# Kernel optimization log

Measured on AMD Instinct MI355X. Metric: run time of the kernel, lower is better.

## Reference

```python
import jax, jax.numpy as jnp
import numpy as np

EMBED_DIM = 256
NUM_HEADS = 8
HEAD_WIDTH = 32
B, L = 2, 2048


def setup_inputs() -> dict:
    key = jax.random.key(0)
    k1, k2, k3, k4 = jax.random.split(key, 4)
    x = jax.random.normal(k1, (B, L, EMBED_DIM), dtype=jnp.float32)
    bias = jax.random.normal(k2, (B, L, L, NUM_HEADS), dtype=jnp.float32)
    # torch Linear weights: [out_features, in_features]
    W_proj = jax.random.normal(k3, (3 * EMBED_DIM, EMBED_DIM), dtype=jnp.float32) * (EMBED_DIM ** -0.5)
    W_o = jax.random.normal(k4, (EMBED_DIM, EMBED_DIM), dtype=jnp.float32) * (EMBED_DIM ** -0.5)
    b_o = jnp.zeros((EMBED_DIM,), dtype=jnp.float32)
    return {"x": x, "bias": bias, "W_proj": W_proj, "W_o": W_o, "b_o": b_o}


def reference(x, bias, W_proj, W_o, b_o):
    b, l, _ = x.shape
    h, hw = NUM_HEADS, HEAD_WIDTH
    # fused QKV projection: (b, l, 3*E)
    t = jnp.einsum('ble,fe->blf', x, W_proj)
    # rearrange '... l (h c) -> ... h l c' with c = 3*hw, then split
    t = t.reshape(b, l, h, 3 * hw).transpose(0, 2, 1, 3)  # (b, h, l, 3*hw)
    q, k, v = jnp.split(t, 3, axis=-1)
    q = q * (hw ** -0.5)
    a = jnp.einsum('bhqc,bhkc->bhqk', q, k)
    a = a + bias.transpose(0, 3, 1, 2)  # (b, h, lq, lk)
    a = jax.nn.softmax(a, axis=-1)
    y = jnp.einsum('bhqk,bhkc->bqhc', a, v)
    y = y.reshape(b, l, h * hw)
    return jnp.einsum('ble,fe->blf', y, W_o) + b_o
```

## Files before the change

### kernel.cpp

```cpp
#include <hip/hip_runtime.h>
#include <math.h>

#define NH   8
#define HW   32
#define LSEQ 2048
#define EMB  256
#define BB   2

typedef short bf16x8 __attribute__((ext_vector_type(8)));
typedef float f32x4  __attribute__((ext_vector_type(4)));

__device__ __forceinline__ unsigned short f2bf(float x) {
  union { float f; unsigned u; } v; v.f = x;
  unsigned r = v.u + 0x7fffu + ((v.u >> 16) & 1u);
  return (unsigned short)(r >> 16);
}
__device__ __forceinline__ float bf2f(unsigned short h) {
  union { float f; unsigned u; } v; v.u = ((unsigned)h) << 16;
  return v.f;
}
__device__ __forceinline__ void split2(float x, unsigned short& h, unsigned short& l) {
  h = f2bf(x);
  l = f2bf(x - bf2f(h));
}

__global__ __launch_bounds__(256, 4) void qkv_gemm(
    const float* __restrict__ X, const float* __restrict__ Wp,
    unsigned short* __restrict__ Qh, unsigned short* __restrict__ Ql,
    unsigned short* __restrict__ Kh, unsigned short* __restrict__ Kl,
    unsigned short* __restrict__ Vth, unsigned short* __restrict__ Vtl) {
  const int t = threadIdx.x;
  const int w = t >> 6, lane = t & 63;
  const int col = lane & 15, quad = lane >> 4;
  const int m0 = blockIdx.y * 64 + w * 16;
  const int n0 = blockIdx.x * 64;
  const float* xrow = X + (size_t)(m0 + col) * 256 + quad * 8;

  f32x4 acc[4];
#pragma unroll
  for (int nt = 0; nt < 4; ++nt) acc[nt] = (f32x4){0.f, 0.f, 0.f, 0.f};

#pragma unroll
  for (int es = 0; es < 8; ++es) {
    float4 xa = *(const float4*)(xrow + es * 32);
    float4 xb = *(const float4*)(xrow + es * 32 + 4);
    float xv[8] = {xa.x, xa.y, xa.z, xa.w, xb.x, xb.y, xb.z, xb.w};
    bf16x8 ah, al;
#pragma unroll
    for (int j = 0; j < 8; ++j) {
      unsigned short hi, lo; split2(xv[j], hi, lo);
      ah[j] = (short)hi; al[j] = (short)lo;
    }
#pragma unroll
    for (int nt = 0; nt < 4; ++nt) {
      const float* wrow = Wp + (size_t)(n0 + nt * 16 + col) * 256 + es * 32 + quad * 8;
      float4 wa = *(const float4*)(wrow);
      float4 wb = *(const float4*)(wrow + 4);
      float wv[8] = {wa.x, wa.y, wa.z, wa.w, wb.x, wb.y, wb.z, wb.w};
      bf16x8 bh, bl;
#pragma unroll
      for (int j = 0; j < 8; ++j) {
        unsigned short hi, lo; split2(wv[j], hi, lo);
        bh[j] = (short)hi; bl[j] = (short)lo;
      }
      acc[nt] = __builtin_amdgcn_mfma_f32_16x16x32_bf16(ah, bh, acc[nt], 0, 0, 0);
      acc[nt] = __builtin_amdgcn_mfma_f32_16x16x32_bf16(ah, bl, acc[nt], 0, 0, 0);
      acc[nt] = __builtin_amdgcn_mfma_f32_16x16x32_bf16(al, bh, acc[nt], 0, 0, 0);
    }
  }

  const float qscale = 0.17677669529663687f;
#pragma unroll
  for (int nt = 0; nt < 4; ++nt) {
    const int f = n0 + nt * 16 + col;
    const int hd = f / 96, r0 = f - hd * 96;
#pragma unroll
    for (int r = 0; r < 4; ++r) {
      const int m = m0 + quad * 4 + r;
      const int bbv = m >> 11, ll = m & 2047;
      float v = acc[nt][r];
      unsigned short hi, lo;
      if (r0 < 64) {
        float sv = (r0 < 32) ? v * qscale : v;
        split2(sv, hi, lo);
        size_t idx = ((size_t)(bbv * NH + hd) * LSEQ + ll) * HW + (r0 & 31);
        if (r0 < 32) { Qh[idx] = hi; Ql[idx] = lo; }
        else         { Kh[idx] = hi; Kl[idx] = lo; }
      } else {
        split2(v, hi, lo);
        size_t idx = ((size_t)(bbv * NH + hd) * HW + (r0 - 64)) * LSEQ + ll;
        Vth[idx] = hi; Vtl[idx] = lo;
      }
    }
  }
}

__global__ __launch_bounds__(512, 4) void attn(
    const unsigned short* __restrict__ Qh, const unsigned short* __restrict__ Ql,
    const unsigned short* __restrict__ Kh, const unsigned short* __restrict__ Kl,
    const unsigned short* __restrict__ Vth, const unsigned short* __restrict__ Vtl,
    const float* __restrict__ Bias, float* __restrict__ Yp,
    float* __restrict__ Mm, float* __restrict__ Ll) {
  __shared__ __attribute__((aligned(16))) float Bst[4 * 32 * 72];
  __shared__ __attribute__((aligned(16))) float Pbuf[8 * 1152];
  const int t = threadIdx.x;
  const int w = t >> 6, lane = t & 63;
  const int col = lane & 15, quad = lane >> 4;
  const int head = w >> 1, wks = w & 1;
  const int x = blockIdx.x;
  const int p = ((x >> 4) << 3) | (x & 7);
  const int hh = (x >> 3) & 1;
  const int ks = p & 1;
  const int b = (p >> 1) & 1;
  const int q0g = (p >> 2) * 32;
  const int hg = hh * 4 + head;
  const int kbase = ks * 1024;

  const size_t bhoff = (size_t)(b * NH + hg) * LSEQ * HW;
  const unsigned short* Qhp = Qh + bhoff;
  const unsigned short* Qlp = Ql + bhoff;
  const unsigned short* Khp = Kh + bhoff;
  const unsigned short* Klp = Kl + bhoff;
  const unsigned short* Vhp = Vth + bhoff;
  const unsigned short* Vlp = Vtl + bhoff;
  float* Pw = &Pbuf[w * 1152];

  bf16x8 Qbh[2], Qbl[2];
#pragma unroll
  for (int qt = 0; qt < 2; ++qt) {
    size_t off = (size_t)(q0g + qt * 16 + col) * HW + quad * 8;
    Qbh[qt] = *(const bf16x8*)(Qhp + off);
    Qbl[qt] = *(const bf16x8*)(Qlp + off);
  }

  f32x4 o[2][2];
#pragma unroll
  for (int ct = 0; ct < 2; ++ct)
#pragma unroll
    for (int qt = 0; qt < 2; ++qt) o[ct][qt] = (f32x4){0.f, 0.f, 0.f, 0.f};
  float m_i[2] = {-1e30f, -1e30f}, l_i[2] = {0.f, 0.f};

  const int sq = w, sk = lane;
  float4 bsr[4];
#pragma unroll
  for (int u = 0; u < 4; ++u)
    bsr[u] = *(const float4*)&Bias[(((size_t)(b * LSEQ + q0g + u * 8 + sq)) * LSEQ +
                                    kbase + sk) * NH + hh * 4];

#pragma unroll 1
  for (int it = 0; it < 16; ++it) {
    __syncthreads();
#pragma unroll
    for (int u = 0; u < 4; ++u) {
      const int qq = u * 8 + sq;
      Bst[0 * 2304 + qq * 72 + sk] = bsr[u].x;
      Bst[1 * 2304 + qq * 72 + sk] = bsr[u].y;
      Bst[2 * 2304 + qq * 72 + sk] = bsr[u].z;
      Bst[3 * 2304 + qq * 72 + sk] = bsr[u].w;
    }
    const int kw = kbase + it * 64 + wks * 32;
    bf16x8 Kah[2], Kal[2], Vah[2], Val[2];
#pragma unroll
    for (int kt = 0; kt < 2; ++kt) {
      size_t off = (size_t)(kw + kt * 16 + col) * HW + quad * 8;
      Kah[kt] = *(const bf16x8*)(Khp + off);
      Kal[kt] = *(const bf16x8*)(Klp + off);
    }
#pragma unroll
    for (int ct = 0; ct < 2; ++ct) {
      size_t off = (size_t)(ct * 16 + col) * LSEQ + kw + quad * 8;
      Vah[ct] = *(const bf16x8*)(Vhp + off);
      Val[ct] = *(const bf16x8*)(Vlp + off);
    }
    if (it < 15) {
#pragma unroll
      for (int u = 0; u < 4; ++u)
        bsr[u] = *(const float4*)&Bias[(((size_t)(b * LSEQ + q0g + u * 8 + sq)) * LSEQ +
                                        kbase + (it + 1) * 64 + sk) * NH + hh * 4];
    }
    __syncthreads();

    f32x4 s[2][2];
#pragma unroll
    for (int kt = 0; kt < 2; ++kt)
#pragma unroll
      for (int qt = 0; qt < 2; ++qt) {
        f32x4 a = *(const f32x4*)&Bst[head * 2304 + (qt * 16 + col) * 72 +
                                      wks * 32 + kt * 16 + quad * 4];
        a = __builtin_amdgcn_mfma_f32_16x16x32_bf16(Kah[kt], Qbh[qt], a, 0, 0, 0);
        a = __builtin_amdgcn_mfma_f32_16x16x32_bf16(Kah[kt], Qbl[qt], a, 0, 0, 0);
        a = __builtin_amdgcn_mfma_f32_16x16x32_bf16(Kal[kt], Qbh[qt], a, 0, 0, 0);
        s[kt][qt] = a;
      }

    float alpha[2];
#pragma unroll
    for (int qt = 0; qt < 2; ++qt) {
      float mx = s[0][qt][0];
#pragma unroll
      for (int r = 1; r < 4; ++r) mx = fmaxf(mx, s[0][qt][r]);
#pragma unroll
      for (int r = 0; r < 4; ++r) mx = fmaxf(mx, s[1][qt][r]);
      mx = fmaxf(mx, __shfl_xor(mx, 16, 64));
      mx = fmaxf(mx, __shfl_xor(mx, 32, 64));
      float mnew = fmaxf(m_i[qt], mx);
      float al = __expf(m_i[qt] - mnew);
      float ps = 0.f;
#pragma unroll
      for (int kt = 0; kt < 2; ++kt)
#pragma unroll
        for (int r = 0; r < 4; ++r) {
          float pv = __expf(s[kt][qt][r] - mnew);
          s[kt][qt][r] = pv;
          ps += pv;
        }
      ps += __shfl_xor(ps, 16, 64);
      ps += __shfl_xor(ps, 32, 64);
      l_i[qt] = l_i[qt] * al + ps;
      m_i[qt] = mnew;
      alpha[qt] = al;
#pragma unroll
      for (int ct = 0; ct < 2; ++ct)
#pragma unroll
        for (int r = 0; r < 4; ++r) o[ct][qt][r] *= al;
    }

#pragma unroll
    for (int kt = 0; kt < 2; ++kt)
#pragma unroll
      for (int qt = 0; qt < 2; ++qt)
#pragma unroll
        for (int r = 0; r < 4; ++r)
          Pw[(kt * 16 + quad * 4 + r) * 34 + qt * 16 + col] = s[kt][qt][r];
    bf16x8 Pbh[2], Pbl[2];
#pragma unroll
    for (int qt = 0; qt < 2; ++qt) {
#pragma unroll
      for (int j = 0; j < 8; ++j) {
        float pv = Pw[(quad * 8 + j) * 34 + qt * 16 + col];
        unsigned short hi, lo; split2(pv, hi, lo);
        Pbh[qt][j] = (short)hi; Pbl[qt][j] = (short)lo;
      }
    }
#pragma unroll
    for (int ct = 0; ct < 2; ++ct)
#pragma unroll
      for (int qt = 0; qt < 2; ++qt) {
        f32x4 a = o[ct][qt];
        a = __builtin_amdgcn_mfma_f32_16x16x32_bf16(Vah[ct], Pbh[qt], a, 0, 0, 0);
        a = __builtin_amdgcn_mfma_f32_16x16x32_bf16(Vah[ct], Pbl[qt], a, 0, 0, 0);
        a = __builtin_amdgcn_mfma_f32_16x16x32_bf16(Val[ct], Pbh[qt], a, 0, 0, 0);
        o[ct][qt] = a;
      }
  }

  __syncthreads();
  if (wks == 1) {
#pragma unroll
    for (int ct = 0; ct < 2; ++ct)
#pragma unroll
      for (int qt = 0; qt < 2; ++qt)
#pragma unroll
        for (int r = 0; r < 4; ++r)
          Pw[(ct * 16 + quad * 4 + r) * 34 + qt * 16 + col] = o[ct][qt][r];
    if (quad == 0) {
#pragma unroll
      for (int qt = 0; qt < 2; ++qt) {
        Pw[1088 + qt * 16 + col] = m_i[qt];
        Pw[1120 + qt * 16 + col] = l_i[qt];
      }
    }
  }
  __syncthreads();
  if (wks == 0) {
    const float* Pp = Pw + 1152;
#pragma unroll
    for (int qt = 0; qt < 2; ++qt) {
      float m2 = Pp[1088 + qt * 16 + col];
      float l2 = Pp[1120 + qt * 16 + col];
      float mm = fmaxf(m_i[qt], m2);
      float a1 = __expf(m_i[qt] - mm);
      float a2 = __expf(m2 - mm);
      float lm = l_i[qt] * a1 + l2 * a2;
      const size_t row = (size_t)ks * 4096 + b * LSEQ + q0g + qt * 16 + col;
      if (quad == 0) {
        Mm[row * 8 + hg] = mm;
        Ll[row * 8 + hg] = lm;
      }
#pragma unroll
      for (int ct = 0; ct < 2; ++ct) {
        float4 res;
        res.x = o[ct][qt][0] * a1 + Pp[(ct * 16 + quad * 4 + 0) * 34 + qt * 16 + col] * a2;
        res.y = o[ct][qt][1] * a1 + Pp[(ct * 16 + quad * 4 + 1) * 34 + qt * 16 + col] * a2;
        res.z = o[ct][qt][2] * a1 + Pp[(ct * 16 + quad * 4 + 2) * 34 + qt * 16 + col] * a2;
        res.w = o[ct][qt][3] * a1 + Pp[(ct * 16 + quad * 4 + 3) * 34 + qt * 16 + col] * a2;
        *(float4*)&Yp[row * EMB + hg * HW + ct * 16 + quad * 4] = res;
      }
    }
  }
}

__global__ __launch_bounds__(256, 4) void out_gemm(
    const float* __restrict__ Yp, const float* __restrict__ Mm,
    const float* __restrict__ Ll, const float* __restrict__ Wo,
    const float* __restrict__ bo, float* __restrict__ Out) {
  const int t = threadIdx.x;
  const int w = t >> 6, lane = t & 63;
  const int col = lane & 15, quad = lane >> 4;
  const int m0 = blockIdx.y * 64 + w * 16;
  const int n0 = blockIdx.x * 64;
  const int grow = m0 + col;
  const float* o1p = Yp + (size_t)grow * 256 + quad * 8;
  const float* o2p = o1p + (size_t)4096 * 256;

  f32x4 acc[4];
#pragma unroll
  for (int nt = 0; nt < 4; ++nt) acc[nt] = (f32x4){0.f, 0.f, 0.f, 0.f};

#pragma unroll
  for (int es = 0; es < 8; ++es) {
    float m1 = Mm[(size_t)grow * 8 + es];
    float l1 = Ll[(size_t)grow * 8 + es];
    float m2 = Mm[(size_t)(4096 + grow) * 8 + es];
    float l2 = Ll[(size_t)(4096 + grow) * 8 + es];
    float M = fmaxf(m1, m2);
    float w1 = __expf(m1 - M), w2 = __expf(m2 - M);
    float inv = 1.0f / (l1 * w1 + l2 * w2);
    w1 *= inv; w2 *= inv;
    float4 a1 = *(const float4*)(o1p + es * 32);
    float4 b1 = *(const float4*)(o1p + es * 32 + 4);
    float4 a2 = *(const float4*)(o2p + es * 32);
    float4 b2 = *(const float4*)(o2p + es * 32 + 4);
    float yv[8] = {a1.x * w1 + a2.x * w2, a1.y * w1 + a2.y * w2,
                   a1.z * w1 + a2.z * w2, a1.w * w1 + a2.w * w2,
                   b1.x * w1 + b2.x * w2, b1.y * w1 + b2.y * w2,
                   b1.z * w1 + b2.z * w2, b1.w * w1 + b2.w * w2};
    bf16x8 ah, al;
#pragma unroll
    for (int j = 0; j < 8; ++j) {
      unsigned short hi, lo; split2(yv[j], hi, lo);
      ah[j] = (short)hi; al[j] = (short)lo;
    }
#pragma unroll
    for (int nt = 0; nt < 4; ++nt) {
      const float* wrow = Wo + (size_t)(n0 + nt * 16 + col) * 256 + es * 32 + quad * 8;
      float4 wa = *(const float4*)(wrow);
      float4 wb = *(const float4*)(wrow + 4);
      float wv[8] = {wa.x, wa.y, wa.z, wa.w, wb.x, wb.y, wb.z, wb.w};
      bf16x8 bh, bl;
#pragma unroll
      for (int j = 0; j < 8; ++j) {
        unsigned short hi, lo; split2(wv[j], hi, lo);
        bh[j] = (short)hi; bl[j] = (short)lo;
      }
      acc[nt] = __builtin_amdgcn_mfma_f32_16x16x32_bf16(ah, bh, acc[nt], 0, 0, 0);
      acc[nt] = __builtin_amdgcn_mfma_f32_16x16x32_bf16(ah, bl, acc[nt], 0, 0, 0);
      acc[nt] = __builtin_amdgcn_mfma_f32_16x16x32_bf16(al, bh, acc[nt], 0, 0, 0);
    }
  }
#pragma unroll
  for (int nt = 0; nt < 4; ++nt) {
    const int f = n0 + nt * 16 + col;
    const float bias_o = bo[f];
#pragma unroll
    for (int r = 0; r < 4; ++r)
      Out[(size_t)(m0 + quad * 4 + r) * 256 + f] = acc[nt][r] + bias_o;
  }
}

extern "C" void kernel_launch(void* const* d_in, const int* in_sizes, int n_in,
                              void* d_out, int out_size, void* d_ws, size_t ws_size,
                              hipStream_t stream) {
  const float* X    = (const float*)d_in[0];
  const float* Bias = (const float*)d_in[1];
  const float* Wp   = (const float*)d_in[2];
  const float* Wo   = (const float*)d_in[3];
  const float* bo   = (const float*)d_in[4];
  float* Out = (float*)d_out;

  const size_t qkv_elems = (size_t)BB * NH * LSEQ * HW;
  unsigned short* Qh  = (unsigned short*)d_ws;
  unsigned short* Ql  = Qh + qkv_elems;
  unsigned short* Kh  = Ql + qkv_elems;
  unsigned short* Kl  = Kh + qkv_elems;
  unsigned short* Vth = Kl + qkv_elems;
  unsigned short* Vtl = Vth + qkv_elems;
  float* Yp = (float*)(Vtl + qkv_elems);
  float* Mm = Yp + (size_t)2 * 4096 * 256;
  float* Ll = Mm + (size_t)2 * 4096 * 8;

  qkv_gemm<<<dim3(12, 64), 256, 0, stream>>>(X, Wp, Qh, Ql, Kh, Kl, Vth, Vtl);
  attn<<<dim3(512), 512, 0, stream>>>(Qh, Ql, Kh, Kl, Vth, Vtl, Bias, Yp, Mm, Ll);
  out_gemm<<<dim3(4, 64), 256, 0, stream>>>(Yp, Mm, Ll, Wo, bo, Out);
}
```

Before: 458.1 us.

## Presplit inputs and weights to bf16 hi/lo once, store P pre-split in LDS

Adds a presplit kernel that converts X, W_proj and W_o into bf16 hi/lo pairs once, so the GEMM kernels load ready-made bf16 vectors instead of redoing the split for every tile. In attention, P is split before being written to LDS as packed hi/lo, and the K/V global loads are issued before the bias LDS stores. out_gemm loads m/l with vector loads hoisted out of the loop. The cost is an extra kernel launch and extra workspace traffic for the split copies.

Result: faster. 448.8 us (-2.0%).

```diff
diff --git a/kernel.cpp b/kernel.cpp
--- a/kernel.cpp
+++ b/kernel.cpp
@@ -9,6 +9,7 @@
 
 typedef short bf16x8 __attribute__((ext_vector_type(8)));
 typedef float f32x4  __attribute__((ext_vector_type(4)));
+typedef unsigned short u16x4 __attribute__((ext_vector_type(4)));
 
 __device__ __forceinline__ unsigned short f2bf(float x) {
   union { float f; unsigned u; } v; v.f = x;
@@ -24,8 +25,37 @@
   l = f2bf(x - bf2f(h));
 }
 
+__global__ __launch_bounds__(256) void presplit(
+    const float* __restrict__ X, const float* __restrict__ Wp,
+    const float* __restrict__ Wo,
+    unsigned short* __restrict__ Xh, unsigned short* __restrict__ Xl,
+    unsigned short* __restrict__ Wph, unsigned short* __restrict__ Wpl,
+    unsigned short* __restrict__ Woh, unsigned short* __restrict__ Wol) {
+  const int NX = 4096 * 256, NP = 768 * 256, NO = 256 * 256;
+  const int total4 = (NX + NP + NO) >> 2;
+  int i4 = blockIdx.x * 256 + threadIdx.x;
+  if (i4 >= total4) return;
+  int e = i4 << 2;
+  const float* src;
+  unsigned short *dh, *dl;
+  int off;
+  if (e < NX)           { src = X;  dh = Xh;  dl = Xl;  off = e; }
+  else if (e < NX + NP) { src = Wp; dh = Wph; dl = Wpl; off = e - NX; }
+  else                  { src = Wo; dh = Woh; dl = Wol; off = e - NX - NP; }
+  float4 v = *(const float4*)(src + off);
+  u16x4 h, l;
+  unsigned short hh, ll;
+  split2(v.x, hh, ll); h[0] = hh; l[0] = ll;
+  split2(v.y, hh, ll); h[1] = hh; l[1] = ll;
+  split2(v.z, hh, ll); h[2] = hh; l[2] = ll;
+  split2(v.w, hh, ll); h[3] = hh; l[3] = ll;
+  *(u16x4*)(dh + off) = h;
+  *(u16x4*)(dl + off) = l;
+}
+
 __global__ __launch_bounds__(256, 4) void qkv_gemm(
-    const float* __restrict__ X, const float* __restrict__ Wp,
+    const unsigned short* __restrict__ Xh, const unsigned short* __restrict__ Xl,
+    const unsigned short* __restrict__ Wph, const unsigned short* __restrict__ Wpl,
     unsigned short* __restrict__ Qh, unsigned short* __restrict__ Ql,
     unsigned short* __restrict__ Kh, unsigned short* __restrict__ Kl,
     unsigned short* __restrict__ Vth, unsigned short* __restrict__ Vtl) {
@@ -34,7 +64,7 @@
   const int col = lane & 15, quad = lane >> 4;
   const int m0 = blockIdx.y * 64 + w * 16;
   const int n0 = blockIdx.x * 64;
-  const float* xrow = X + (size_t)(m0 + col) * 256 + quad * 8;
+  const size_t xoff = (size_t)(m0 + col) * 256 + quad * 8;
 
   f32x4 acc[4];
 #pragma unroll
@@ -42,27 +72,13 @@
 
 #pragma unroll
   for (int es = 0; es < 8; ++es) {
-    float4 xa = *(const float4*)(xrow + es * 32);
-    float4 xb = *(const float4*)(xrow + es * 32 + 4);
-    float xv[8] = {xa.x, xa.y, xa.z, xa.w, xb.x, xb.y, xb.z, xb.w};
-    bf16x8 ah, al;
-#pragma unroll
-    for (int j = 0; j < 8; ++j) {
-      unsigned short hi, lo; split2(xv[j], hi, lo);
-      ah[j] = (short)hi; al[j] = (short)lo;
-    }
+    bf16x8 ah = *(const bf16x8*)(Xh + xoff + es * 32);
+    bf16x8 al = *(const bf16x8*)(Xl + xoff + es * 32);
 #pragma unroll
     for (int nt = 0; nt < 4; ++nt) {
-      const float* wrow = Wp + (size_t)(n0 + nt * 16 + col) * 256 + es * 32 + quad * 8;
-      float4 wa = *(const float4*)(wrow);
-      float4 wb = *(const float4*)(wrow + 4);
-      float wv[8] = {wa.x, wa.y, wa.z, wa.w, wb.x, wb.y, wb.z, wb.w};
-      bf16x8 bh, bl;
-#pragma unroll
-      for (int j = 0; j < 8; ++j) {
-        unsigned short hi, lo; split2(wv[j], hi, lo);
-        bh[j] = (short)hi; bl[j] = (short)lo;
-      }
+      const size_t woff = (size_t)(n0 + nt * 16 + col) * 256 + es * 32 + quad * 8;
+      bf16x8 bh = *(const bf16x8*)(Wph + woff);
+      bf16x8 bl = *(const bf16x8*)(Wpl + woff);
       acc[nt] = __builtin_amdgcn_mfma_f32_16x16x32_bf16(ah, bh, acc[nt], 0, 0, 0);
       acc[nt] = __builtin_amdgcn_mfma_f32_16x16x32_bf16(ah, bl, acc[nt], 0, 0, 0);
       acc[nt] = __builtin_amdgcn_mfma_f32_16x16x32_bf16(al, bh, acc[nt], 0, 0, 0);
@@ -102,7 +118,7 @@
     const float* __restrict__ Bias, float* __restrict__ Yp,
     float* __restrict__ Mm, float* __restrict__ Ll) {
   __shared__ __attribute__((aligned(16))) float Bst[4 * 32 * 72];
-  __shared__ __attribute__((aligned(16))) float Pbuf[8 * 1152];
+  __shared__ __attribute__((aligned(16))) unsigned Pbuf[8 * 1152];
   const int t = threadIdx.x;
   const int w = t >> 6, lane = t & 63;
   const int col = lane & 15, quad = lane >> 4;
@@ -123,7 +139,7 @@
   const unsigned short* Klp = Kl + bhoff;
   const unsigned short* Vhp = Vth + bhoff;
   const unsigned short* Vlp = Vtl + bhoff;
-  float* Pw = &Pbuf[w * 1152];
+  unsigned* Pw = &Pbuf[w * 1152];
 
   bf16x8 Qbh[2], Qbl[2];
 #pragma unroll
@@ -150,6 +166,20 @@
 #pragma unroll 1
   for (int it = 0; it < 16; ++it) {
     __syncthreads();
+    const int kw = kbase + it * 64 + wks * 32;
+    bf16x8 Kah[2], Kal[2], Vah[2], Val[2];
+#pragma unroll
+    for (int kt = 0; kt < 2; ++kt) {
+      size_t off = (size_t)(kw + kt * 16 + col) * HW + quad * 8;
+      Kah[kt] = *(const bf16x8*)(Khp + off);
+      Kal[kt] = *(const bf16x8*)(Klp + off);
+    }
+#pragma unroll
+    for (int ct = 0; ct < 2; ++ct) {
+      size_t off = (size_t)(ct * 16 + col) * LSEQ + kw + quad * 8;
+      Vah[ct] = *(const bf16x8*)(Vhp + off);
+      Val[ct] = *(const bf16x8*)(Vlp + off);
+    }
 #pragma unroll
     for (int u = 0; u < 4; ++u) {
       const int qq = u * 8 + sq;
@@ -157,20 +187,6 @@
       Bst[1 * 2304 + qq * 72 + sk] = bsr[u].y;
       Bst[2 * 2304 + qq * 72 + sk] = bsr[u].z;
       Bst[3 * 2304 + qq * 72 + sk] = bsr[u].w;
-    }
-    const int kw = kbase + it * 64 + wks * 32;
-    bf16x8 Kah[2], Kal[2], Vah[2], Val[2];
-#pragma unroll
-    for (int kt = 0; kt < 2; ++kt) {
-      size_t off = (size_t)(kw + kt * 16 + col) * HW + quad * 8;
-      Kah[kt] = *(const bf16x8*)(Khp + off);
-      Kal[kt] = *(const bf16x8*)(Klp + off);
-    }
-#pragma unroll
-    for (int ct = 0; ct < 2; ++ct) {
-      size_t off = (size_t)(ct * 16 + col) * LSEQ + kw + quad * 8;
-      Vah[ct] = *(const bf16x8*)(Vhp + off);
-      Val[ct] = *(const bf16x8*)(Vlp + off);
     }
     if (it < 15) {
 #pragma unroll
@@ -230,16 +246,19 @@
 #pragma unroll
       for (int qt = 0; qt < 2; ++qt)
 #pragma unroll
-        for (int r = 0; r < 4; ++r)
-          Pw[(kt * 16 + quad * 4 + r) * 34 + qt * 16 + col] = s[kt][qt][r];
+        for (int r = 0; r < 4; ++r) {
+          unsigned short hi, lo; split2(s[kt][qt][r], hi, lo);
+          Pw[(kt * 16 + quad * 4 + r) * 34 + qt * 16 + col] =
+              (unsigned)hi | ((unsigned)lo << 16);
+        }
     bf16x8 Pbh[2], Pbl[2];
 #pragma unroll
     for (int qt = 0; qt < 2; ++qt) {
 #pragma unroll
       for (int j = 0; j < 8; ++j) {
-        float pv = Pw[(quad * 8 + j) * 34 + qt * 16 + col];
-        unsigned short hi, lo; split2(pv, hi, lo);
-        Pbh[qt][j] = (short)hi; Pbl[qt][j] = (short)lo;
+        unsigned d = Pw[(quad * 8 + j) * 34 + qt * 16 + col];
+        Pbh[qt][j] = (short)(d & 0xffffu);
+        Pbl[qt][j] = (short)(d >> 16);
       }
     }
 #pragma unroll
@@ -255,6 +274,7 @@
   }
 
   __syncthreads();
+  float* Pwf = (float*)Pw;
   if (wks == 1) {
 #pragma unroll
     for (int ct = 0; ct < 2; ++ct)
@@ -262,18 +282,18 @@
       for (int qt = 0; qt < 2; ++qt)
 #pragma unroll
         for (int r = 0; r < 4; ++r)
-          Pw[(ct * 16 + quad * 4 + r) * 34 + qt * 16 + col] = o[ct][qt][r];
+          Pwf[(ct * 16 + quad * 4 + r) * 34 + qt * 16 + col] = o[ct][qt][r];
     if (quad == 0) {
 #pragma unroll
       for (int qt = 0; qt < 2; ++qt) {
-        Pw[1088 + qt * 16 + col] = m_i[qt];
-        Pw[1120 + qt * 16 + col] = l_i[qt];
+        Pwf[1088 + qt * 16 + col] = m_i[qt];
+        Pwf[1120 + qt * 16 + col] = l_i[qt];
       }
     }
   }
   __syncthreads();
   if (wks == 0) {
-    const float* Pp = Pw + 1152;
+    const float* Pp = Pwf + 1152;
 #pragma unroll
     for (int qt = 0; qt < 2; ++qt) {
       float m2 = Pp[1088 + qt * 16 + col];
@@ -302,8 +322,9 @@
 
 __global__ __launch_bounds__(256, 4) void out_gemm(
     const float* __restrict__ Yp, const float* __restrict__ Mm,
-    const float* __restrict__ Ll, const float* __restrict__ Wo,
-    const float* __restrict__ bo, float* __restrict__ Out) {
+    const float* __restrict__ Ll, const unsigned short* __restrict__ Woh,
+    const unsigned short* __restrict__ Wol, const float* __restrict__ bo,
+    float* __restrict__ Out) {
   const int t = threadIdx.x;
   const int w = t >> 6, lane = t & 63;
   const int col = lane & 15, quad = lane >> 4;
@@ -313,19 +334,25 @@
   const float* o1p = Yp + (size_t)grow * 256 + quad * 8;
   const float* o2p = o1p + (size_t)4096 * 256;
 
+  float m1v[8], l1v[8], m2v[8], l2v[8];
+  *(float4*)&m1v[0] = *(const float4*)&Mm[(size_t)grow * 8];
+  *(float4*)&m1v[4] = *(const float4*)&Mm[(size_t)grow * 8 + 4];
+  *(float4*)&l1v[0] = *(const float4*)&Ll[(size_t)grow * 8];
+  *(float4*)&l1v[4] = *(const float4*)&Ll[(size_t)grow * 8 + 4];
+  *(float4*)&m2v[0] = *(const float4*)&Mm[(size_t)(4096 + grow) * 8];
+  *(float4*)&m2v[4] = *(const float4*)&Mm[(size_t)(4096 + grow) * 8 + 4];
+  *(float4*)&l2v[0] = *(const float4*)&Ll[(size_t)(4096 + grow) * 8];
+  *(float4*)&l2v[4] = *(const float4*)&Ll[(size_t)(4096 + grow) * 8 + 4];
+
   f32x4 acc[4];
 #pragma unroll
   for (int nt = 0; nt < 4; ++nt) acc[nt] = (f32x4){0.f, 0.f, 0.f, 0.f};
 
 #pragma unroll
   for (int es = 0; es < 8; ++es) {
-    float m1 = Mm[(size_t)grow * 8 + es];
-    float l1 = Ll[(size_t)grow * 8 + es];
-    float m2 = Mm[(size_t)(4096 + grow) * 8 + es];
-    float l2 = Ll[(size_t)(4096 + grow) * 8 + es];
-    float M = fmaxf(m1, m2);
-    float w1 = __expf(m1 - M), w2 = __expf(m2 - M);
-    float inv = 1.0f / (l1 * w1 + l2 * w2);
+    float M = fmaxf(m1v[es], m2v[es]);
+    float w1 = __expf(m1v[es] - M), w2 = __expf(m2v[es] - M);
+    float inv = 1.0f / (l1v[es] * w1 + l2v[es] * w2);
     w1 *= inv; w2 *= inv;
     float4 a1 = *(const float4*)(o1p + es * 32);
     float4 b1 = *(const float4*)(o1p + es * 32 + 4);
@@ -343,16 +370,9 @@
     }
 #pragma unroll
     for (int nt = 0; nt < 4; ++nt) {
-      const float* wrow = Wo + (size_t)(n0 + nt * 16 + col) * 256 + es * 32 + quad * 8;
-      float4 wa = *(const float4*)(wrow);
-      float4 wb = *(const float4*)(wrow + 4);
-      float wv[8] = {wa.x, wa.y, wa.z, wa.w, wb.x, wb.y, wb.z, wb.w};
-      bf16x8 bh, bl;
-#pragma unroll
-      for (int j = 0; j < 8; ++j) {
-        unsigned short hi, lo; split2(wv[j], hi, lo);
-        bh[j] = (short)hi; bl[j] = (short)lo;
-      }
+      const size_t woff = (size_t)(n0 + nt * 16 + col) * 256 + es * 32 + quad * 8;
+      bf16x8 bh = *(const bf16x8*)(Woh + woff);
+      bf16x8 bl = *(const bf16x8*)(Wol + woff);
       acc[nt] = __builtin_amdgcn_mfma_f32_16x16x32_bf16(ah, bh, acc[nt], 0, 0, 0);
       acc[nt] = __builtin_amdgcn_mfma_f32_16x16x32_bf16(ah, bl, acc[nt], 0, 0, 0);
       acc[nt] = __builtin_amdgcn_mfma_f32_16x16x32_bf16(al, bh, acc[nt], 0, 0, 0);
@@ -388,8 +408,15 @@
   float* Yp = (float*)(Vtl + qkv_elems);
   float* Mm = Yp + (size_t)2 * 4096 * 256;
   float* Ll = Mm + (size_t)2 * 4096 * 8;
-
-  qkv_gemm<<<dim3(12, 64), 256, 0, stream>>>(X, Wp, Qh, Ql, Kh, Kl, Vth, Vtl);
+  unsigned short* Xh  = (unsigned short*)(Ll + (size_t)2 * 4096 * 8);
+  unsigned short* Xl  = Xh  + (size_t)4096 * 256;
+  unsigned short* Wph = Xl  + (size_t)4096 * 256;
+  unsigned short* Wpl = Wph + (size_t)768 * 256;
+  unsigned short* Woh = Wpl + (size_t)768 * 256;
+  unsigned short* Wol = Woh + (size_t)256 * 256;
+
+  presplit<<<dim3(1280), 256, 0, stream>>>(X, Wp, Wo, Xh, Xl, Wph, Wpl, Woh, Wol);
+  qkv_gemm<<<dim3(12, 64), 256, 0, stream>>>(Xh, Xl, Wph, Wpl, Qh, Ql, Kh, Kl, Vth, Vtl);
   attn<<<dim3(512), 512, 0, stream>>>(Qh, Ql, Kh, Kl, Vth, Vtl, Bias, Yp, Mm, Ll);
-  out_gemm<<<dim3(4, 64), 256, 0, stream>>>(Yp, Mm, Ll, Wo, bo, Out);
-}
+  out_gemm<<<dim3(4, 64), 256, 0, stream>>>(Yp, Mm, Ll, Woh, Wol, bo, Out);
+}
```
